# Kernel optimization log

Measured on AMD Instinct MI355X. Metric: run time of the kernel, lower is better.

## Reference

```python
import jax, jax.numpy as jnp
import numpy as np

N, C, A = 4096, 1000, 2048


def setup_inputs() -> dict:
    key = jax.random.key(0)
    k1, k2, k3, k4 = jax.random.split(key, 4)
    features = jax.random.normal(k1, (N, A), dtype=jnp.float32)
    labels = jax.random.randint(k2, (N,), 0, C, dtype=jnp.int64)
    cv_matrix = jax.random.uniform(k3, (N, A), dtype=jnp.float32)
    ratio = jnp.asarray(0.5, dtype=jnp.float32)
    weight = jax.random.normal(k4, (C, A), dtype=jnp.float32) * 0.02
    bias = jnp.zeros((C,), dtype=jnp.float32)
    return {"features": features, "labels": labels, "cv_matrix": cv_matrix,
            "ratio": ratio, "weight": weight, "bias": bias}


def reference(features, labels, cv_matrix, ratio, weight, bias):
    # logits = features @ W^T + b
    logits = features @ weight.T + bias  # [N, C]
    # sigma2[n,c] = ratio * sum_a (W[c,a] - W[y_n,a])^2 * cv[n,a]
    # Expand the square to avoid materializing the [N, C, A] tensor:
    #   = sum_a W[c,a]^2 cv - 2 sum_a W[c,a] (W[y,a] cv) + sum_a W[y,a]^2 cv
    Wy = weight[labels]                          # [N, A] gather of per-label rows
    t1 = cv_matrix @ (weight * weight).T         # [N, C]
    t2 = (cv_matrix * Wy) @ weight.T             # [N, C]
    t3 = jnp.sum(Wy * Wy * cv_matrix, axis=1, keepdims=True)  # [N, 1]
    sigma2 = ratio * (t1 - 2.0 * t2 + t3)        # [N, C]
    aug_logits = logits + 0.5 * sigma2
    # mean cross-entropy on augmented logits
    logp = jax.nn.log_softmax(aug_logits, axis=-1)
    nll = -jnp.take_along_axis(logp, labels[:, None], axis=1)[:, 0]
    loss = jnp.mean(nll)
    return loss, logits
```

## Files before the change

kernel.cpp:

```cpp
#include <hip/hip_runtime.h>
#include <hip/hip_bf16.h>

#define N_ROWS 4096
#define C_CLS  1000
#define C_PAD  1024
#define A_DIM  2048

typedef __attribute__((ext_vector_type(8))) short short8;
typedef __attribute__((ext_vector_type(4))) float f32x4;

__device__ __forceinline__ unsigned short f2bf(float x) {
    unsigned u = __float_as_uint(x);
    unsigned rounding = 0x7fffu + ((u >> 16) & 1u);
    return (unsigned short)((u + rounding) >> 16);
}

__device__ __forceinline__ unsigned pack2(float a, float b) {
    return (unsigned)f2bf(a) | ((unsigned)f2bf(b) << 16);
}

__global__ __launch_bounds__(256) void prep_w(const float* __restrict__ W,
                                              unsigned short* __restrict__ Wb,
                                              unsigned short* __restrict__ W2b) {
    int t = blockIdx.x * 256 + threadIdx.x;
    int a4 = t * 4;
    int c = a4 >> 11;
    int a = a4 & (A_DIM - 1);
    float4 w = make_float4(0.f, 0.f, 0.f, 0.f);
    if (c < C_CLS) w = *(const float4*)(W + (size_t)c * A_DIM + a);
    uint2 pw, pw2;
    pw.x  = pack2(w.x, w.y);             pw.y  = pack2(w.z, w.w);
    pw2.x = pack2(w.x * w.x, w.y * w.y); pw2.y = pack2(w.z * w.z, w.w * w.w);
    *(uint2*)(Wb  + (size_t)a4) = pw;
    *(uint2*)(W2b + (size_t)a4) = pw2;
}

__global__ __launch_bounds__(256) void prep_a(const float* __restrict__ F,
                                              const float* __restrict__ CV,
                                              const float* __restrict__ W,
                                              const int* __restrict__ labels,
                                              const float* __restrict__ ratio_p,
                                              unsigned short* __restrict__ Fb,
                                              unsigned short* __restrict__ Ub,
                                              unsigned short* __restrict__ Vb,
                                              float* __restrict__ t3c) {
    int n = blockIdx.x;
    int y = labels[n];
    float ratio = ratio_p[0];
    float hr = 0.5f * ratio;
    const float* frow  = F  + (size_t)n * A_DIM;
    const float* cvrow = CV + (size_t)n * A_DIM;
    const float* wyrow = W  + (size_t)y * A_DIM;
    size_t obase = (size_t)n * A_DIM;
    float s = 0.f;
    #pragma unroll
    for (int seg = 0; seg < 2; seg++) {
        int a = (threadIdx.x + seg * 256) * 4;
        float4 f  = *(const float4*)(frow + a);
        float4 cv = *(const float4*)(cvrow + a);
        float4 wy = *(const float4*)(wyrow + a);
        float u0 = f.x - ratio * cv.x * wy.x;
        float u1 = f.y - ratio * cv.y * wy.y;
        float u2 = f.z - ratio * cv.z * wy.z;
        float u3 = f.w - ratio * cv.w * wy.w;
        s += wy.x * wy.x * cv.x + wy.y * wy.y * cv.y
           + wy.z * wy.z * cv.z + wy.w * wy.w * cv.w;
        uint2 pf, pu, pv;
        pf.x = pack2(f.x, f.y);               pf.y = pack2(f.z, f.w);
        pu.x = pack2(u0, u1);                 pu.y = pack2(u2, u3);
        pv.x = pack2(hr * cv.x, hr * cv.y);   pv.y = pack2(hr * cv.z, hr * cv.w);
        *(uint2*)(Fb + obase + a) = pf;
        *(uint2*)(Ub + obase + a) = pu;
        *(uint2*)(Vb + obase + a) = pv;
    }
    for (int off = 32; off; off >>= 1) s += __shfl_down(s, off);
    __shared__ float wsum[4];
    int lane = threadIdx.x & 63, wid = threadIdx.x >> 6;
    if (lane == 0) wsum[wid] = s;
    __syncthreads();
    if (threadIdx.x == 0)
        t3c[n] = hr * (wsum[0] + wsum[1] + wsum[2] + wsum[3]);
}

#define BM 128
#define BN 128
#define BK 32
#define LDSP 40

__global__ __launch_bounds__(512) void gemm_fused(
        const unsigned short* __restrict__ Fb, const unsigned short* __restrict__ Ub,
        const unsigned short* __restrict__ Vb, const unsigned short* __restrict__ Wb,
        const unsigned short* __restrict__ W2b,
        const float* __restrict__ t3c, const float* __restrict__ bias,
        float* __restrict__ out_logits, float* __restrict__ aug) {
    __shared__ unsigned short sF[BM * LDSP];
    __shared__ unsigned short sU[BM * LDSP];
    __shared__ unsigned short sV[BM * LDSP];
    __shared__ unsigned short sW[BN * LDSP];
    __shared__ unsigned short sW2[BN * LDSP];

    int bn = blockIdx.x, bm = blockIdx.y;
    int tid = threadIdx.x;
    int lane = tid & 63, wid = tid >> 6;
    int wm = wid >> 2, wn = wid & 3;

    int sr = tid >> 2;
    int sc = (tid & 3) * 8;
    size_t gA = (size_t)(bm * BM + sr) * A_DIM + sc;
    size_t gB = (size_t)(bn * BN + sr) * A_DIM + sc;
    int sdst = sr * LDSP + sc;

    f32x4 accL[4][2] = {};
    f32x4 accA[4][2] = {};

    int fr_row = lane & 15;
    int fr_k   = (lane >> 4) * 8;

    for (int k0 = 0; k0 < A_DIM; k0 += BK) {
        uint4 vF  = *(const uint4*)(Fb  + gA + k0);
        uint4 vU  = *(const uint4*)(Ub  + gA + k0);
        uint4 vV  = *(const uint4*)(Vb  + gA + k0);
        uint4 vW  = *(const uint4*)(Wb  + gB + k0);
        uint4 vW2 = *(const uint4*)(W2b + gB + k0);
        __syncthreads();
        *(uint4*)(sF  + sdst) = vF;
        *(uint4*)(sU  + sdst) = vU;
        *(uint4*)(sV  + sdst) = vV;
        *(uint4*)(sW  + sdst) = vW;
        *(uint4*)(sW2 + sdst) = vW2;
        __syncthreads();

        short8 aF[4], aU[4], aV[4], bW[2], bW2[2];
        #pragma unroll
        for (int m = 0; m < 4; m++) {
            int row = wm * 64 + m * 16 + fr_row;
            aF[m] = *(const short8*)(sF + row * LDSP + fr_k);
            aU[m] = *(const short8*)(sU + row * LDSP + fr_k);
            aV[m] = *(const short8*)(sV + row * LDSP + fr_k);
        }
        #pragma unroll
        for (int n = 0; n < 2; n++) {
            int row = wn * 32 + n * 16 + fr_row;
            bW[n]  = *(const short8*)(sW  + row * LDSP + fr_k);
            bW2[n] = *(const short8*)(sW2 + row * LDSP + fr_k);
        }
        #pragma unroll
        for (int m = 0; m < 4; m++)
            #pragma unroll
            for (int n = 0; n < 2; n++) {
                accL[m][n] = __builtin_amdgcn_mfma_f32_16x16x32_bf16(aF[m], bW[n],  accL[m][n], 0, 0, 0);
                accA[m][n] = __builtin_amdgcn_mfma_f32_16x16x32_bf16(aU[m], bW[n],  accA[m][n], 0, 0, 0);
                accA[m][n] = __builtin_amdgcn_mfma_f32_16x16x32_bf16(aV[m], bW2[n], accA[m][n], 0, 0, 0);
            }
    }

    #pragma unroll
    for (int n = 0; n < 2; n++) {
        int col = bn * BN + wn * 32 + n * 16 + (lane & 15);
        if (col >= C_CLS) continue;
        float bv = bias[col];
        #pragma unroll
        for (int m = 0; m < 4; m++) {
            int rbase = bm * BM + wm * 64 + m * 16 + (lane >> 4) * 4;
            #pragma unroll
            for (int j = 0; j < 4; j++) {
                int row = rbase + j;
                out_logits[(size_t)row * C_CLS + col] = accL[m][n][j] + bv;
                aug[(size_t)row * C_PAD + col] = accA[m][n][j] + bv + t3c[row];
            }
        }
    }
}

__global__ __launch_bounds__(256) void softmax_nll(const float* __restrict__ aug,
                                                   const int* __restrict__ labels,
                                                   float* __restrict__ nll) {
    int n = blockIdx.x;
    const float* row = aug + (size_t)n * C_PAD;
    int lane = threadIdx.x & 63, wid = threadIdx.x >> 6;
    __shared__ float sm[4], ss[4];

    float mx = -1e30f;
    for (int c = threadIdx.x; c < C_CLS; c += 256) mx = fmaxf(mx, row[c]);
    for (int off = 32; off; off >>= 1) mx = fmaxf(mx, __shfl_down(mx, off));
    if (lane == 0) sm[wid] = mx;
    __syncthreads();
    mx = fmaxf(fmaxf(sm[0], sm[1]), fmaxf(sm[2], sm[3]));

    float s = 0.f;
    for (int c = threadIdx.x; c < C_CLS; c += 256) s += __expf(row[c] - mx);
    for (int off = 32; off; off >>= 1) s += __shfl_down(s, off);
    if (lane == 0) ss[wid] = s;
    __syncthreads();
    if (threadIdx.x == 0) {
        float tot = ss[0] + ss[1] + ss[2] + ss[3];
        nll[n] = logf(tot) + mx - row[labels[n]];
    }
}

__global__ __launch_bounds__(256) void final_reduce(const float* __restrict__ nll,
                                                    float* __restrict__ out_loss) {
    float s = 0.f;
    for (int i = threadIdx.x; i < N_ROWS; i += 256) s += nll[i];
    for (int off = 32; off; off >>= 1) s += __shfl_down(s, off);
    __shared__ float ss[4];
    int lane = threadIdx.x & 63, wid = threadIdx.x >> 6;
    if (lane == 0) ss[wid] = s;
    __syncthreads();
    if (threadIdx.x == 0)
        out_loss[0] = (ss[0] + ss[1] + ss[2] + ss[3]) / (float)N_ROWS;
}

extern "C" void kernel_launch(void* const* d_in, const int* in_sizes, int n_in,
                              void* d_out, int out_size, void* d_ws, size_t ws_size,
                              hipStream_t stream) {
    const float* features = (const float*)d_in[0];
    const int*   labels   = (const int*)d_in[1];
    const float* cv       = (const float*)d_in[2];
    const float* ratio    = (const float*)d_in[3];
    const float* weight   = (const float*)d_in[4];
    const float* bias     = (const float*)d_in[5];
    float* out = (float*)d_out;

    char* p = (char*)d_ws;
    unsigned short* Wb  = (unsigned short*)p; p += (size_t)C_PAD * A_DIM * 2;
    unsigned short* W2b = (unsigned short*)p; p += (size_t)C_PAD * A_DIM * 2;
    unsigned short* Fb  = (unsigned short*)p; p += (size_t)N_ROWS * A_DIM * 2;
    unsigned short* Ub  = (unsigned short*)p; p += (size_t)N_ROWS * A_DIM * 2;
    unsigned short* Vb  = (unsigned short*)p; p += (size_t)N_ROWS * A_DIM * 2;
    float* t3c   = (float*)p; p += (size_t)N_ROWS * 4;
    float* aug   = (float*)p; p += (size_t)N_ROWS * C_PAD * 4;
    float* nllb  = (float*)p; p += (size_t)N_ROWS * 4;

    prep_w<<<(C_PAD * A_DIM / 4) / 256, 256, 0, stream>>>(weight, Wb, W2b);
    prep_a<<<N_ROWS, 256, 0, stream>>>(features, cv, weight, labels, ratio,
                                       Fb, Ub, Vb, t3c);
    gemm_fused<<<dim3(C_PAD / BN, N_ROWS / BM), 512, 0, stream>>>(
        Fb, Ub, Vb, Wb, W2b, t3c, bias, out + 1, aug);
    softmax_nll<<<N_ROWS, 256, 0, stream>>>(aug, labels, nllb);
    final_reduce<<<1, 256, 0, stream>>>(nllb, out);
}
```

Before: 232.8 us.

## Merge prep kernels, use direct-to-LDS loads with swizzle, XCD-aware GEMM tiling, atomic loss

Fuses the weight and activation prep kernels into one launch with 8-wide vectorised conversions. The GEMM now uses global_load_lds to copy tiles straight into XOR-swizzled LDS without register staging. It also moves to a 128x64 tile with 256 threads and two blocks per CU, and remaps block IDs so tiles sharing a weight column land on the same XCD. The final reduction kernel is replaced by per-row atomicAdd into the loss, which removes a launch but makes the summation order nondeterministic.

```diff
diff --git a/kernel.cpp b/kernel.cpp
--- a/kernel.cpp
+++ b/kernel.cpp
@@ -19,32 +19,44 @@
     return (unsigned)f2bf(a) | ((unsigned)f2bf(b) << 16);
 }
 
-__global__ __launch_bounds__(256) void prep_w(const float* __restrict__ W,
-                                              unsigned short* __restrict__ Wb,
-                                              unsigned short* __restrict__ W2b) {
-    int t = blockIdx.x * 256 + threadIdx.x;
-    int a4 = t * 4;
-    int c = a4 >> 11;
-    int a = a4 & (A_DIM - 1);
-    float4 w = make_float4(0.f, 0.f, 0.f, 0.f);
-    if (c < C_CLS) w = *(const float4*)(W + (size_t)c * A_DIM + a);
-    uint2 pw, pw2;
-    pw.x  = pack2(w.x, w.y);             pw.y  = pack2(w.z, w.w);
-    pw2.x = pack2(w.x * w.x, w.y * w.y); pw2.y = pack2(w.z * w.z, w.w * w.w);
-    *(uint2*)(Wb  + (size_t)a4) = pw;
-    *(uint2*)(W2b + (size_t)a4) = pw2;
-}
-
-__global__ __launch_bounds__(256) void prep_a(const float* __restrict__ F,
-                                              const float* __restrict__ CV,
-                                              const float* __restrict__ W,
-                                              const int* __restrict__ labels,
-                                              const float* __restrict__ ratio_p,
-                                              unsigned short* __restrict__ Fb,
-                                              unsigned short* __restrict__ Ub,
-                                              unsigned short* __restrict__ Vb,
-                                              float* __restrict__ t3c) {
-    int n = blockIdx.x;
+__device__ __forceinline__ void gload16(unsigned short* lds, const unsigned short* g) {
+    __builtin_amdgcn_global_load_lds(
+        (const __attribute__((address_space(1))) unsigned int*)g,
+        (__attribute__((address_space(3))) unsigned int*)lds,
+        16, 0, 0);
+}
+
+__global__ __launch_bounds__(256) void prep_all(
+        const float* __restrict__ F, const float* __restrict__ CV,
+        const float* __restrict__ W, const int* __restrict__ labels,
+        const float* __restrict__ ratio_p,
+        unsigned short* __restrict__ Fb, unsigned short* __restrict__ Ub,
+        unsigned short* __restrict__ Vb,
+        unsigned short* __restrict__ Wb, unsigned short* __restrict__ W2b,
+        float* __restrict__ t3c, float* __restrict__ out_loss) {
+    int bid = blockIdx.x;
+    if (bid >= N_ROWS) {
+        if (bid == N_ROWS && threadIdx.x == 0) out_loss[0] = 0.f;
+        int t = (bid - N_ROWS) * 256 + threadIdx.x;
+        int a8 = t * 8;
+        int c = a8 >> 11;
+        int a = a8 & (A_DIM - 1);
+        float4 w0 = make_float4(0.f, 0.f, 0.f, 0.f);
+        float4 w1 = make_float4(0.f, 0.f, 0.f, 0.f);
+        if (c < C_CLS) {
+            w0 = *(const float4*)(W + (size_t)c * A_DIM + a);
+            w1 = *(const float4*)(W + (size_t)c * A_DIM + a + 4);
+        }
+        uint4 pw, pw2;
+        pw.x  = pack2(w0.x, w0.y);  pw.y  = pack2(w0.z, w0.w);
+        pw.z  = pack2(w1.x, w1.y);  pw.w  = pack2(w1.z, w1.w);
+        pw2.x = pack2(w0.x*w0.x, w0.y*w0.y);  pw2.y = pack2(w0.z*w0.z, w0.w*w0.w);
+        pw2.z = pack2(w1.x*w1.x, w1.y*w1.y);  pw2.w = pack2(w1.z*w1.z, w1.w*w1.w);
+        *(uint4*)(Wb  + (size_t)a8) = pw;
+        *(uint4*)(W2b + (size_t)a8) = pw2;
+        return;
+    }
+    int n = bid;
     int y = labels[n];
     float ratio = ratio_p[0];
     float hr = 0.5f * ratio;
@@ -52,27 +64,31 @@
     const float* cvrow = CV + (size_t)n * A_DIM;
     const float* wyrow = W  + (size_t)y * A_DIM;
     size_t obase = (size_t)n * A_DIM;
-    float s = 0.f;
-    #pragma unroll
-    for (int seg = 0; seg < 2; seg++) {
-        int a = (threadIdx.x + seg * 256) * 4;
-        float4 f  = *(const float4*)(frow + a);
-        float4 cv = *(const float4*)(cvrow + a);
-        float4 wy = *(const float4*)(wyrow + a);
-        float u0 = f.x - ratio * cv.x * wy.x;
-        float u1 = f.y - ratio * cv.y * wy.y;
-        float u2 = f.z - ratio * cv.z * wy.z;
-        float u3 = f.w - ratio * cv.w * wy.w;
-        s += wy.x * wy.x * cv.x + wy.y * wy.y * cv.y
-           + wy.z * wy.z * cv.z + wy.w * wy.w * cv.w;
-        uint2 pf, pu, pv;
-        pf.x = pack2(f.x, f.y);               pf.y = pack2(f.z, f.w);
-        pu.x = pack2(u0, u1);                 pu.y = pack2(u2, u3);
-        pv.x = pack2(hr * cv.x, hr * cv.y);   pv.y = pack2(hr * cv.z, hr * cv.w);
-        *(uint2*)(Fb + obase + a) = pf;
-        *(uint2*)(Ub + obase + a) = pu;
-        *(uint2*)(Vb + obase + a) = pv;
-    }
+
+    int a = threadIdx.x * 8;
+    float4 f0  = *(const float4*)(frow + a);
+    float4 f1  = *(const float4*)(frow + a + 4);
+    float4 c0  = *(const float4*)(cvrow + a);
+    float4 c1  = *(const float4*)(cvrow + a + 4);
+    float4 y0  = *(const float4*)(wyrow + a);
+    float4 y1  = *(const float4*)(wyrow + a + 4);
+
+    float s = y0.x*y0.x*c0.x + y0.y*y0.y*c0.y + y0.z*y0.z*c0.z + y0.w*y0.w*c0.w
+            + y1.x*y1.x*c1.x + y1.y*y1.y*c1.y + y1.z*y1.z*c1.z + y1.w*y1.w*c1.w;
+
+    uint4 pf, pu, pv;
+    pf.x = pack2(f0.x, f0.y);  pf.y = pack2(f0.z, f0.w);
+    pf.z = pack2(f1.x, f1.y);  pf.w = pack2(f1.z, f1.w);
+    pu.x = pack2(f0.x - ratio*c0.x*y0.x, f0.y - ratio*c0.y*y0.y);
+    pu.y = pack2(f0.z - ratio*c0.z*y0.z, f0.w - ratio*c0.w*y0.w);
+    pu.z = pack2(f1.x - ratio*c1.x*y1.x, f1.y - ratio*c1.y*y1.y);
+    pu.w = pack2(f1.z - ratio*c1.z*y1.z, f1.w - ratio*c1.w*y1.w);
+    pv.x = pack2(hr*c0.x, hr*c0.y);  pv.y = pack2(hr*c0.z, hr*c0.w);
+    pv.z = pack2(hr*c1.x, hr*c1.y);  pv.w = pack2(hr*c1.z, hr*c1.w);
+    *(uint4*)(Fb + obase + a) = pf;
+    *(uint4*)(Ub + obase + a) = pu;
+    *(uint4*)(Vb + obase + a) = pv;
+
     for (int off = 32; off; off >>= 1) s += __shfl_down(s, off);
     __shared__ float wsum[4];
     int lane = threadIdx.x & 63, wid = threadIdx.x >> 6;
@@ -83,90 +99,93 @@
 }
 
 #define BM 128
-#define BN 128
+#define BN 64
 #define BK 32
-#define LDSP 40
-
-__global__ __launch_bounds__(512) void gemm_fused(
+
+__global__ __launch_bounds__(256, 2) void gemm_fused(
         const unsigned short* __restrict__ Fb, const unsigned short* __restrict__ Ub,
         const unsigned short* __restrict__ Vb, const unsigned short* __restrict__ Wb,
         const unsigned short* __restrict__ W2b,
         const float* __restrict__ t3c, const float* __restrict__ bias,
         float* __restrict__ out_logits, float* __restrict__ aug) {
-    __shared__ unsigned short sF[BM * LDSP];
-    __shared__ unsigned short sU[BM * LDSP];
-    __shared__ unsigned short sV[BM * LDSP];
-    __shared__ unsigned short sW[BN * LDSP];
-    __shared__ unsigned short sW2[BN * LDSP];
-
-    int bn = blockIdx.x, bm = blockIdx.y;
+    __shared__ unsigned short sF[BM * BK];
+    __shared__ unsigned short sU[BM * BK];
+    __shared__ unsigned short sV[BM * BK];
+    __shared__ unsigned short sW[BN * BK];
+    __shared__ unsigned short sW2[BN * BK];
+
+    int wg = blockIdx.x;
+    int xcd = wg & 7, idx = wg >> 3;
+    int bn = (xcd << 1) | (idx >> 5);
+    int bm = idx & 31;
+
     int tid = threadIdx.x;
     int lane = tid & 63, wid = tid >> 6;
-    int wm = wid >> 2, wn = wid & 3;
-
-    int sr = tid >> 2;
-    int sc = (tid & 3) * 8;
-    size_t gA = (size_t)(bm * BM + sr) * A_DIM + sc;
-    size_t gB = (size_t)(bn * BN + sr) * A_DIM + sc;
-    int sdst = sr * LDSP + sc;
+    int wm = wid >> 1, wn = wid & 1;
+
+    int srow = lane >> 2;
+    int scs = ((lane & 3) * 8) ^ (((srow >> 1) & 3) << 3);
+    int r0 = wid * 16 + srow;
+    size_t ga0 = (size_t)(bm * BM + r0) * A_DIM + scs;
+    size_t ga1 = ga0 + (size_t)64 * A_DIM;
+    size_t gb  = (size_t)(bn * BN + r0) * A_DIM + scs;
+    int d0 = wid * 512;
+    int d1 = 2048 + wid * 512;
+
+    int fr = lane & 15;
+    int kof = ((lane >> 4) * 8) ^ (((fr >> 1) & 3) << 3);
+    int aoff = fr * BK + kof;
 
     f32x4 accL[4][2] = {};
     f32x4 accA[4][2] = {};
 
-    int fr_row = lane & 15;
-    int fr_k   = (lane >> 4) * 8;
-
     for (int k0 = 0; k0 < A_DIM; k0 += BK) {
-        uint4 vF  = *(const uint4*)(Fb  + gA + k0);
-        uint4 vU  = *(const uint4*)(Ub  + gA + k0);
-        uint4 vV  = *(const uint4*)(Vb  + gA + k0);
-        uint4 vW  = *(const uint4*)(Wb  + gB + k0);
-        uint4 vW2 = *(const uint4*)(W2b + gB + k0);
         __syncthreads();
-        *(uint4*)(sF  + sdst) = vF;
-        *(uint4*)(sU  + sdst) = vU;
-        *(uint4*)(sV  + sdst) = vV;
-        *(uint4*)(sW  + sdst) = vW;
-        *(uint4*)(sW2 + sdst) = vW2;
+        gload16(sF + d0, Fb + ga0);   gload16(sF + d1, Fb + ga1);
+        gload16(sU + d0, Ub + ga0);   gload16(sU + d1, Ub + ga1);
+        gload16(sV + d0, Vb + ga0);   gload16(sV + d1, Vb + ga1);
+        gload16(sW + d0, Wb + gb);    gload16(sW2 + d0, W2b + gb);
+        ga0 += BK; ga1 += BK; gb += BK;
         __syncthreads();
 
-        short8 aF[4], aU[4], aV[4], bW[2], bW2[2];
+        short8 aF[4], aU[4], aV[4], bWf[2], bW2f[2];
         #pragma unroll
         for (int m = 0; m < 4; m++) {
-            int row = wm * 64 + m * 16 + fr_row;
-            aF[m] = *(const short8*)(sF + row * LDSP + fr_k);
-            aU[m] = *(const short8*)(sU + row * LDSP + fr_k);
-            aV[m] = *(const short8*)(sV + row * LDSP + fr_k);
+            int off = wm * 2048 + m * 512 + aoff;
+            aF[m] = *(const short8*)(sF + off);
+            aU[m] = *(const short8*)(sU + off);
+            aV[m] = *(const short8*)(sV + off);
         }
         #pragma unroll
         for (int n = 0; n < 2; n++) {
-            int row = wn * 32 + n * 16 + fr_row;
-            bW[n]  = *(const short8*)(sW  + row * LDSP + fr_k);
-            bW2[n] = *(const short8*)(sW2 + row * LDSP + fr_k);
+            int off = wn * 1024 + n * 512 + aoff;
+            bWf[n]  = *(const short8*)(sW + off);
+            bW2f[n] = *(const short8*)(sW2 + off);
         }
         #pragma unroll
         for (int m = 0; m < 4; m++)
             #pragma unroll
             for (int n = 0; n < 2; n++) {
-                accL[m][n] = __builtin_amdgcn_mfma_f32_16x16x32_bf16(aF[m], bW[n],  accL[m][n], 0, 0, 0);
-                accA[m][n] = __builtin_amdgcn_mfma_f32_16x16x32_bf16(aU[m], bW[n],  accA[m][n], 0, 0, 0);
-                accA[m][n] = __builtin_amdgcn_mfma_f32_16x16x32_bf16(aV[m], bW2[n], accA[m][n], 0, 0, 0);
+                accL[m][n] = __builtin_amdgcn_mfma_f32_16x16x32_bf16(aF[m], bWf[n],  accL[m][n], 0, 0, 0);
+                accA[m][n] = __builtin_amdgcn_mfma_f32_16x16x32_bf16(aU[m], bWf[n],  accA[m][n], 0, 0, 0);
+                accA[m][n] = __builtin_amdgcn_mfma_f32_16x16x32_bf16(aV[m], bW2f[n], accA[m][n], 0, 0, 0);
             }
     }
 
     #pragma unroll
     for (int n = 0; n < 2; n++) {
-        int col = bn * BN + wn * 32 + n * 16 + (lane & 15);
-        if (col >= C_CLS) continue;
-        float bv = bias[col];
-        #pragma unroll
-        for (int m = 0; m < 4; m++) {
-            int rbase = bm * BM + wm * 64 + m * 16 + (lane >> 4) * 4;
+        int col = bn * BN + wn * 32 + n * 16 + fr;
+        if (col < C_CLS) {
+            float bv = bias[col];
             #pragma unroll
-            for (int j = 0; j < 4; j++) {
-                int row = rbase + j;
-                out_logits[(size_t)row * C_CLS + col] = accL[m][n][j] + bv;
-                aug[(size_t)row * C_PAD + col] = accA[m][n][j] + bv + t3c[row];
+            for (int m = 0; m < 4; m++) {
+                int rbase = bm * BM + wm * 64 + m * 16 + (lane >> 4) * 4;
+                #pragma unroll
+                for (int j = 0; j < 4; j++) {
+                    int row = rbase + j;
+                    out_logits[(size_t)row * C_CLS + col] = accL[m][n][j] + bv;
+                    aug[(size_t)row * C_PAD + col] = accA[m][n][j] + bv + t3c[row];
+                }
             }
         }
     }
@@ -174,7 +193,7 @@
 
 __global__ __launch_bounds__(256) void softmax_nll(const float* __restrict__ aug,
                                                    const int* __restrict__ labels,
-                                                   float* __restrict__ nll) {
+                                                   float* __restrict__ out_loss) {
     int n = blockIdx.x;
     const float* row = aug + (size_t)n * C_PAD;
     int lane = threadIdx.x & 63, wid = threadIdx.x >> 6;
@@ -194,21 +213,9 @@
     __syncthreads();
     if (threadIdx.x == 0) {
         float tot = ss[0] + ss[1] + ss[2] + ss[3];
-        nll[n] = logf(tot) + mx - row[labels[n]];
-    }
-}
-
-__global__ __launch_bounds__(256) void final_reduce(const float* __restrict__ nll,
-                                                    float* __restrict__ out_loss) {
-    float s = 0.f;
-    for (int i = threadIdx.x; i < N_ROWS; i += 256) s += nll[i];
-    for (int off = 32; off; off >>= 1) s += __shfl_down(s, off);
-    __shared__ float ss[4];
-    int lane = threadIdx.x & 63, wid = threadIdx.x >> 6;
-    if (lane == 0) ss[wid] = s;
-    __syncthreads();
-    if (threadIdx.x == 0)
-        out_loss[0] = (ss[0] + ss[1] + ss[2] + ss[3]) / (float)N_ROWS;
+        float nll = logf(tot) + mx - row[labels[n]];
+        atomicAdd(out_loss, nll * (1.0f / (float)N_ROWS));
+    }
 }
 
 extern "C" void kernel_launch(void* const* d_in, const int* in_sizes, int n_in,
@@ -228,15 +235,13 @@
     unsigned short* Fb  = (unsigned short*)p; p += (size_t)N_ROWS * A_DIM * 2;
     unsigned short* Ub  = (unsigned short*)p; p += (size_t)N_ROWS * A_DIM * 2;
     unsigned short* Vb  = (unsigned short*)p; p += (size_t)N_ROWS * A_DIM * 2;
-    float* t3c   = (float*)p; p += (size_t)N_ROWS * 4;
-    float* aug   = (float*)p; p += (size_t)N_ROWS * C_PAD * 4;
-    float* nllb  = (float*)p; p += (size_t)N_ROWS * 4;
-
-    prep_w<<<(C_PAD * A_DIM / 4) / 256, 256, 0, stream>>>(weight, Wb, W2b);
-    prep_a<<<N_ROWS, 256, 0, stream>>>(features, cv, weight, labels, ratio,
-                                       Fb, Ub, Vb, t3c);
-    gemm_fused<<<dim3(C_PAD / BN, N_ROWS / BM), 512, 0, stream>>>(
+    float* t3c = (float*)p; p += (size_t)N_ROWS * 4;
+    float* aug = (float*)p; p += (size_t)N_ROWS * C_PAD * 4;
+
+    int wprep_blocks = (C_PAD * A_DIM / 8) / 256;
+    prep_all<<<N_ROWS + wprep_blocks, 256, 0, stream>>>(
+        features, cv, weight, labels, ratio, Fb, Ub, Vb, Wb, W2b, t3c, out);
+    gemm_fused<<<(C_PAD / BN) * (N_ROWS / BM), 256, 0, stream>>>(
         Fb, Ub, Vb, Wb, W2b, t3c, bias, out + 1, aug);
-    softmax_nll<<<N_ROWS, 256, 0, stream>>>(aug, labels, nllb);
-    final_reduce<<<1, 256, 0, stream>>>(nllb, out);
-}
+    softmax_nll<<<N_ROWS, 256, 0, stream>>>(aug, labels, out);
+}
```

Measured after the change: 270.6 us. 16.2% more time.
